# Kernel optimization log

Hardware: AMD Instinct MI355X
Metric: run time of the kernel (lower is better)

Reference implementation:

```python
import jax, jax.numpy as jnp
import numpy as np

B, L, D, H = 2, 2048, 1024, 16
DH = D // H  # 64

def setup_inputs() -> dict:
    key = jax.random.key(0)
    ks = jax.random.split(key, 5)
    s = 1.0 / np.sqrt(D)
    return {
        "x": jax.random.normal(ks[0], (B, L, D), jnp.float32),
        "Wk": jax.random.normal(ks[1], (D, D), jnp.float32) * s,
        "Wq": jax.random.normal(ks[2], (D, D), jnp.float32) * s,
        "Wv": jax.random.normal(ks[3], (D, D), jnp.float32) * s,
        "Wo": jax.random.normal(ks[4], (D, D), jnp.float32) * s,
    }

def reference(x, Wk, Wq, Wv, Wo):
    # Linear(D,D,bias=False): y = x @ W.T ; W stored [out,in] as in torch
    k = (x @ Wk.T).reshape(B, L, H, DH).transpose(0, 2, 1, 3)  # [B,H,L,dh]
    q = (x @ Wq.T).reshape(B, L, H, DH).transpose(0, 2, 1, 3)
    v = (x @ Wv.T).reshape(B, L, H, DH).transpose(0, 2, 1, 3)
    att = jnp.einsum("bhqd,bhkd->bhqk", q, k) / jnp.sqrt(jnp.float32(DH))
    causal = jnp.tril(jnp.ones((L, L), dtype=bool))
    att = jnp.where(causal, att, -jnp.inf)
    p = jax.nn.softmax(att, axis=-1)  # dropout omitted (eval mode)
    out = jnp.einsum("bhqk,bhkd->bhqd", p, v)  # [B,H,L,dh]
    out = out.transpose(0, 2, 1, 3).reshape(B, L, D)
    return out @ Wo.T
```

## Files before the change

kernel.cpp:

```cpp
#include <hip/hip_runtime.h>

typedef __bf16 bf16_t;
typedef __bf16 bf16x8 __attribute__((ext_vector_type(8)));
typedef __bf16 bf16x4 __attribute__((ext_vector_type(4)));
typedef float f32x4 __attribute__((ext_vector_type(4)));

#define MFMA_BF16(a, b, c) __builtin_amdgcn_mfma_f32_16x16x32_bf16((a), (b), (c), 0, 0, 0)

__device__ __forceinline__ void gload16(const bf16_t* g, bf16_t* l) {
  __builtin_amdgcn_global_load_lds(
      (__attribute__((address_space(1))) void*)(g),
      (__attribute__((address_space(3))) void*)(l), 16, 0, 0);
}

__global__ void cast_all(const float* __restrict__ x, const float* __restrict__ wk,
                         const float* __restrict__ wq, const float* __restrict__ wv,
                         const float* __restrict__ wo, bf16_t* __restrict__ xbf,
                         bf16_t* __restrict__ wbf) {
  const size_t NX = 4194304, NW = 1048576;
  size_t i = (size_t)blockIdx.x * blockDim.x + threadIdx.x;
  const size_t total4 = (NX + 4 * NW) / 4;
  const size_t stride = (size_t)gridDim.x * blockDim.x;
  for (; i < total4; i += stride) {
    size_t f = i * 4;
    const float* src;
    bf16_t* dst;
    if (f < NX) {
      src = x + f;
      dst = xbf + f;
    } else {
      size_t g = f - NX;
      size_t wsel = g >> 20;
      size_t off = g & (NW - 1);
      dst = wbf + g;
      src = (wsel == 0) ? wq + off : (wsel == 1) ? wk + off : (wsel == 2) ? wv + off : wo + off;
    }
    float4 v = *(const float4*)src;
    bf16x4 o;
    o[0] = (bf16_t)v.x; o[1] = (bf16_t)v.y; o[2] = (bf16_t)v.z; o[3] = (bf16_t)v.w;
    *(bf16x4*)dst = o;
  }
}

template <typename TOUT>
__global__ __launch_bounds__(256) void gemm_nt(const bf16_t* __restrict__ A,
                                               const bf16_t* __restrict__ W,
                                               TOUT* __restrict__ C, int K, int ldc,
                                               int blocksPerSect, bf16_t* __restrict__ vtb) {
  __shared__ bf16_t As[128 * 32];
  __shared__ bf16_t Bs[128 * 32];
  const int t = threadIdx.x;
  const int l = t & 63, w = t >> 6;
  const int wm = w >> 1, wn = w & 1;
  const int lr = l & 15, lg = l >> 4;
  const int bm = blockIdx.x;
  const int by = blockIdx.y;
  const int sect = by / blocksPerSect;
  const int bn = by - sect * blocksPerSect;
  const bf16_t* Wp = W + ((size_t)sect << 20);
  const int n0 = sect * 1024 + bn * 128;

  const bf16_t* ag = A + (size_t)(bm * 128 + (t >> 2)) * K + (t & 3) * 8;
  const bf16_t* bg = Wp + (size_t)(bn * 128 + (t >> 2)) * K + (t & 3) * 8;
  const size_t rs64 = (size_t)64 * K;

  f32x4 acc[4][4];
#pragma unroll
  for (int i = 0; i < 4; ++i)
#pragma unroll
    for (int j = 0; j < 4; ++j) acc[i][j] = (f32x4){0.f, 0.f, 0.f, 0.f};

  for (int k0 = 0; k0 < K; k0 += 32) {
    __syncthreads();
    gload16(ag, As + t * 8);
    gload16(ag + rs64, As + 2048 + t * 8);
    gload16(bg, Bs + t * 8);
    gload16(bg + rs64, Bs + 2048 + t * 8);
    ag += 32;
    bg += 32;
    __syncthreads();
    bf16x8 af[4], bfr[4];
#pragma unroll
    for (int mf = 0; mf < 4; ++mf)
      af[mf] = *(const bf16x8*)(As + (wm * 64 + mf * 16 + lr) * 32 + lg * 8);
#pragma unroll
    for (int nf = 0; nf < 4; ++nf)
      bfr[nf] = *(const bf16x8*)(Bs + (wn * 64 + nf * 16 + lr) * 32 + lg * 8);
#pragma unroll
    for (int mf = 0; mf < 4; ++mf)
#pragma unroll
      for (int nf = 0; nf < 4; ++nf)
        acc[mf][nf] = MFMA_BF16(af[mf], bfr[nf], acc[mf][nf]);
  }

  if (vtb != nullptr && sect == 2) {
#pragma unroll
    for (int mf = 0; mf < 4; ++mf)
#pragma unroll
      for (int nf = 0; nf < 4; ++nf) {
        int row0 = bm * 128 + wm * 64 + mf * 16 + lg * 4;
        int colg = bn * 128 + wn * 64 + nf * 16 + lr;
        int bb = row0 >> 11, ll = row0 & 2047;
        size_t vaddr = ((size_t)((bb * 16 + (colg >> 6)) * 64 + (colg & 63))) * 2048 + ll;
        bf16x4 pk;
#pragma unroll
        for (int j = 0; j < 4; ++j) pk[j] = (bf16_t)acc[mf][nf][j];
        *(bf16x4*)(vtb + vaddr) = pk;
      }
  } else {
#pragma unroll
    for (int mf = 0; mf < 4; ++mf)
#pragma unroll
      for (int nf = 0; nf < 4; ++nf)
#pragma unroll
        for (int j = 0; j < 4; ++j) {
          int row = bm * 128 + wm * 64 + mf * 16 + lg * 4 + j;
          int col = n0 + wn * 64 + nf * 16 + lr;
          C[(size_t)row * ldc + col] = (TOUT)acc[mf][nf][j];
        }
  }
}

__global__ __launch_bounds__(256) void attn_fwd(const bf16_t* __restrict__ qk,
                                                const bf16_t* __restrict__ vt,
                                                bf16_t* __restrict__ out) {
  __shared__ bf16_t Ks[64 * 64];
  __shared__ bf16_t Vts[64 * 64];
  __shared__ bf16_t Pt[4][16 * 72];
  const int t = threadIdx.x, l = t & 63, w = t >> 6;
  const int lr = l & 15, lg = l >> 4;
  const int bh = blockIdx.x;
  const int b = bh >> 4, h = bh & 15;
  const int qt = (int)(gridDim.y - 1) - (int)blockIdx.y;
  const int qrow = qt * 64 + w * 16 + lr;

  const bf16_t* Qg = qk + (size_t)(b * 2048 + qrow) * 2048 + h * 64 + lg * 8;
  bf16x8 qf0 = *(const bf16x8*)(Qg);
  bf16x8 qf1 = *(const bf16x8*)(Qg + 32);
#pragma unroll
  for (int j = 0; j < 8; ++j) {
    qf0[j] = (bf16_t)((float)qf0[j] * 0.125f);
    qf1[j] = (bf16_t)((float)qf1[j] * 0.125f);
  }

  f32x4 acc_o[4];
#pragma unroll
  for (int df = 0; df < 4; ++df) acc_o[df] = (f32x4){0.f, 0.f, 0.f, 0.f};
  float m_r = -1e30f, l_r = 0.f;
  bf16_t* Pw = &Pt[w][0];

  const int srow = t >> 3;
  const int sc8 = t & 7;

  for (int kt = 0; kt <= qt; ++kt) {
    __syncthreads();
#pragma unroll
    for (int r = 0; r < 2; ++r) {
      int row = r * 32 + srow;
      int cs = sc8 ^ (row & 7);
      gload16(qk + (size_t)(b * 2048 + kt * 64 + row) * 2048 + 1024 + h * 64 + cs * 8,
              Ks + (r * 256 + t) * 8);
      gload16(vt + ((size_t)(bh * 64 + row)) * 2048 + kt * 64 + cs * 8,
              Vts + (r * 256 + t) * 8);
    }
    __syncthreads();

    f32x4 sc[4];
#pragma unroll
    for (int nf = 0; nf < 4; ++nf) sc[nf] = (f32x4){0.f, 0.f, 0.f, 0.f};
#pragma unroll
    for (int nf = 0; nf < 4; ++nf) {
      int row = nf * 16 + lr;
      int r7 = row & 7;
      bf16x8 kf0 = *(const bf16x8*)(Ks + row * 64 + ((lg ^ r7) * 8));
      bf16x8 kf1 = *(const bf16x8*)(Ks + row * 64 + (((lg ^ 4) ^ r7) * 8));
      sc[nf] = MFMA_BF16(kf0, qf0, sc[nf]);
      sc[nf] = MFMA_BF16(kf1, qf1, sc[nf]);
    }
    float s[16];
#pragma unroll
    for (int nf = 0; nf < 4; ++nf)
#pragma unroll
      for (int j = 0; j < 4; ++j) s[nf * 4 + j] = sc[nf][j];
    if (kt == qt) {
      const int qloc = w * 16 + lr;
#pragma unroll
      for (int nf = 0; nf < 4; ++nf)
#pragma unroll
        for (int j = 0; j < 4; ++j)
          if (nf * 16 + lg * 4 + j > qloc) s[nf * 4 + j] = -1e30f;
    }

    float m16 = s[0];
#pragma unroll
    for (int i = 1; i < 16; ++i) m16 = fmaxf(m16, s[i]);
    float rm = fmaxf(m16, __shfl_xor(m16, 16));
    rm = fmaxf(rm, __shfl_xor(rm, 32));
    float mnew = fmaxf(m_r, rm);
    float sf = __expf(m_r - mnew);
    m_r = mnew;
    float p[16], ps = 0.f;
#pragma unroll
    for (int i = 0; i < 16; ++i) {
      p[i] = __expf(s[i] - mnew);
      ps += p[i];
    }
    ps += __shfl_xor(ps, 16);
    ps += __shfl_xor(ps, 32);
    l_r = l_r * sf + ps;
#pragma unroll
    for (int df = 0; df < 4; ++df)
#pragma unroll
      for (int j = 0; j < 4; ++j) acc_o[df][j] *= sf;

#pragma unroll
    for (int nf = 0; nf < 4; ++nf) {
      bf16x4 pk;
#pragma unroll
      for (int j = 0; j < 4; ++j) pk[j] = (bf16_t)p[nf * 4 + j];
      *(bf16x4*)(Pw + lr * 72 + nf * 16 + lg * 4) = pk;
    }

    bf16x8 pb0 = *(const bf16x8*)(Pw + lr * 72 + lg * 8);
    bf16x8 pb1 = *(const bf16x8*)(Pw + lr * 72 + 32 + lg * 8);
#pragma unroll
    for (int df = 0; df < 4; ++df) {
      int arow = df * 16 + lr;
      int r7 = arow & 7;
      bf16x8 vf0 = *(const bf16x8*)(Vts + arow * 64 + ((lg ^ r7) * 8));
      bf16x8 vf1 = *(const bf16x8*)(Vts + arow * 64 + (((lg ^ 4) ^ r7) * 8));
      acc_o[df] = MFMA_BF16(vf0, pb0, acc_o[df]);
      acc_o[df] = MFMA_BF16(vf1, pb1, acc_o[df]);
    }
  }

  float inv = 1.f / l_r;
#pragma unroll
  for (int df = 0; df < 4; ++df) {
    bf16x4 o;
#pragma unroll
    for (int j = 0; j < 4; ++j) o[j] = (bf16_t)(acc_o[df][j] * inv);
    *(bf16x4*)(out + (size_t)(b * 2048 + qrow) * 1024 + h * 64 + df * 16 + lg * 4) = o;
  }
}

extern "C" void kernel_launch(void* const* d_in, const int* in_sizes, int n_in,
                              void* d_out, int out_size, void* d_ws, size_t ws_size,
                              hipStream_t stream) {
  const float* x = (const float*)d_in[0];
  const float* wk = (const float*)d_in[1];
  const float* wq = (const float*)d_in[2];
  const float* wv = (const float*)d_in[3];
  const float* wo = (const float*)d_in[4];

  bf16_t* xbf = (bf16_t*)d_ws;
  bf16_t* wbf = xbf + 4194304;
  bf16_t* qkbf = wbf + 4194304;
  bf16_t* vtbuf = qkbf + 8388608;
  bf16_t* attnbf = xbf;
  float* out = (float*)d_out;

  cast_all<<<dim3(2048), dim3(256), 0, stream>>>(x, wk, wq, wv, wo, xbf, wbf);
  gemm_nt<bf16_t><<<dim3(32, 24), dim3(256), 0, stream>>>(xbf, wbf, qkbf, 1024, 2048, 8, vtbuf);
  attn_fwd<<<dim3(32, 32), dim3(256), 0, stream>>>(qkbf, vtbuf, attnbf);
  gemm_nt<float><<<dim3(32, 8), dim3(256), 0, stream>>>(attnbf, wbf + 3 * 1048576, out, 1024,
                                                        1024, 8, (bf16_t*)nullptr);
}
```

Measured before the change: 120.1 us.

## Pair causal query tiles per block, double-buffer K/V, and lazily rescale softmax

Each attention block now handles two query tiles (qt and 31-qt), so every block does the same amount of causal work and K/V tiles loaded into LDS serve both query tiles while they overlap. K/V loads are double-buffered so the next tile's global-to-LDS copy runs during the current tile's compute, with one barrier per iteration instead of two. The online softmax skips rescaling the accumulators unless the row max grows by more than a threshold. The trade-off is half as many blocks, with more registers and LDS per block.

```diff
diff --git a/kernel.cpp b/kernel.cpp
--- a/kernel.cpp
+++ b/kernel.cpp
@@ -121,126 +121,174 @@
   }
 }
 
+template <int NP>
+__device__ __forceinline__ void attn_tile(const bf16_t* Kb, const bf16_t* Vb, bf16_t* Pw,
+                                          const bf16x8 (&qf)[2][2], f32x4 (&acc)[2][4],
+                                          float (&m_r)[2], float (&l_r)[2], int qloc,
+                                          const int (&diag)[2], int lr, int lg) {
+  f32x4 sc[2][4];
+#pragma unroll
+  for (int pp = 0; pp < NP; ++pp)
+#pragma unroll
+    for (int nf = 0; nf < 4; ++nf) sc[pp][nf] = (f32x4){0.f, 0.f, 0.f, 0.f};
+#pragma unroll
+  for (int nf = 0; nf < 4; ++nf) {
+    int row = nf * 16 + lr, r7 = row & 7;
+    bf16x8 kf0 = *(const bf16x8*)(Kb + row * 64 + (lg ^ r7) * 8);
+    bf16x8 kf1 = *(const bf16x8*)(Kb + row * 64 + ((lg ^ 4) ^ r7) * 8);
+#pragma unroll
+    for (int pp = 0; pp < NP; ++pp) {
+      sc[pp][nf] = MFMA_BF16(kf0, qf[pp][0], sc[pp][nf]);
+      sc[pp][nf] = MFMA_BF16(kf1, qf[pp][1], sc[pp][nf]);
+    }
+  }
+#pragma unroll
+  for (int pp = 0; pp < NP; ++pp) {
+    float s[16];
+#pragma unroll
+    for (int nf = 0; nf < 4; ++nf)
+#pragma unroll
+      for (int j = 0; j < 4; ++j) s[nf * 4 + j] = sc[pp][nf][j];
+    if (diag[pp]) {
+#pragma unroll
+      for (int nf = 0; nf < 4; ++nf)
+#pragma unroll
+        for (int j = 0; j < 4; ++j)
+          if (nf * 16 + lg * 4 + j > qloc) s[nf * 4 + j] = -1e30f;
+    }
+    float t0 = fmaxf(fmaxf(s[0], s[1]), fmaxf(s[2], s[3]));
+    float t1 = fmaxf(fmaxf(s[4], s[5]), fmaxf(s[6], s[7]));
+    float t2 = fmaxf(fmaxf(s[8], s[9]), fmaxf(s[10], s[11]));
+    float t3 = fmaxf(fmaxf(s[12], s[13]), fmaxf(s[14], s[15]));
+    float m16 = fmaxf(fmaxf(t0, t1), fmaxf(t2, t3));
+    float rm = fmaxf(m16, __shfl_xor(m16, 16));
+    rm = fmaxf(rm, __shfl_xor(rm, 32));
+    if (!__all(rm - m_r[pp] <= 8.f)) {
+      float mnew = fmaxf(m_r[pp], rm);
+      float sf = __expf(m_r[pp] - mnew);
+      m_r[pp] = mnew;
+      l_r[pp] *= sf;
+#pragma unroll
+      for (int df = 0; df < 4; ++df)
+#pragma unroll
+        for (int j = 0; j < 4; ++j) acc[pp][df][j] *= sf;
+    }
+    float p[16], ps = 0.f;
+#pragma unroll
+    for (int i = 0; i < 16; ++i) {
+      p[i] = __expf(s[i] - m_r[pp]);
+      ps += p[i];
+    }
+    ps += __shfl_xor(ps, 16);
+    ps += __shfl_xor(ps, 32);
+    l_r[pp] += ps;
+#pragma unroll
+    for (int nf = 0; nf < 4; ++nf) {
+      bf16x4 pk;
+#pragma unroll
+      for (int j = 0; j < 4; ++j) pk[j] = (bf16_t)p[nf * 4 + j];
+      *(bf16x4*)(Pw + pp * 1152 + lr * 72 + nf * 16 + lg * 4) = pk;
+    }
+  }
+  bf16x8 pb[2][2];
+#pragma unroll
+  for (int pp = 0; pp < NP; ++pp) {
+    pb[pp][0] = *(const bf16x8*)(Pw + pp * 1152 + lr * 72 + lg * 8);
+    pb[pp][1] = *(const bf16x8*)(Pw + pp * 1152 + lr * 72 + 32 + lg * 8);
+  }
+#pragma unroll
+  for (int df = 0; df < 4; ++df) {
+    int arow = df * 16 + lr, r7 = arow & 7;
+    bf16x8 vf0 = *(const bf16x8*)(Vb + arow * 64 + (lg ^ r7) * 8);
+    bf16x8 vf1 = *(const bf16x8*)(Vb + arow * 64 + ((lg ^ 4) ^ r7) * 8);
+#pragma unroll
+    for (int pp = 0; pp < NP; ++pp) {
+      acc[pp][df] = MFMA_BF16(vf0, pb[pp][0], acc[pp][df]);
+      acc[pp][df] = MFMA_BF16(vf1, pb[pp][1], acc[pp][df]);
+    }
+  }
+}
+
 __global__ __launch_bounds__(256) void attn_fwd(const bf16_t* __restrict__ qk,
                                                 const bf16_t* __restrict__ vt,
                                                 bf16_t* __restrict__ out) {
-  __shared__ bf16_t Ks[64 * 64];
-  __shared__ bf16_t Vts[64 * 64];
-  __shared__ bf16_t Pt[4][16 * 72];
+  __shared__ bf16_t Ks[2][4096];
+  __shared__ bf16_t Vts[2][4096];
+  __shared__ bf16_t Pt[4][2304];
   const int t = threadIdx.x, l = t & 63, w = t >> 6;
   const int lr = l & 15, lg = l >> 4;
   const int bh = blockIdx.x;
   const int b = bh >> 4, h = bh & 15;
-  const int qt = (int)(gridDim.y - 1) - (int)blockIdx.y;
-  const int qrow = qt * 64 + w * 16 + lr;
-
-  const bf16_t* Qg = qk + (size_t)(b * 2048 + qrow) * 2048 + h * 64 + lg * 8;
-  bf16x8 qf0 = *(const bf16x8*)(Qg);
-  bf16x8 qf1 = *(const bf16x8*)(Qg + 32);
-#pragma unroll
-  for (int j = 0; j < 8; ++j) {
-    qf0[j] = (bf16_t)((float)qf0[j] * 0.125f);
-    qf1[j] = (bf16_t)((float)qf1[j] * 0.125f);
-  }
-
-  f32x4 acc_o[4];
-#pragma unroll
-  for (int df = 0; df < 4; ++df) acc_o[df] = (f32x4){0.f, 0.f, 0.f, 0.f};
-  float m_r = -1e30f, l_r = 0.f;
+  const int pr = blockIdx.y;
+  const int qlo = pr, qhi = 31 - pr;
+  const int qtile[2] = {qhi, qlo};
+  const int qloc = w * 16 + lr;
+
+  const int srow = t >> 3, sc8 = t & 7;
+  const int cs = sc8 ^ (srow & 7);
+  const bf16_t* kbase = qk + ((size_t)(b * 2048 + srow)) * 2048 + 1024 + h * 64 + cs * 8;
+  const bf16_t* vbase = vt + ((size_t)(bh * 64 + srow)) * 2048 + cs * 8;
   bf16_t* Pw = &Pt[w][0];
 
-  const int srow = t >> 3;
-  const int sc8 = t & 7;
-
-  for (int kt = 0; kt <= qt; ++kt) {
+#define STAGE(ktile, buf)                                              \
+  do {                                                                 \
+    const bf16_t* ks_ = kbase + (size_t)(ktile) * (64 * 2048);         \
+    const bf16_t* vs_ = vbase + (size_t)(ktile) * 64;                  \
+    gload16(ks_, &Ks[buf][t * 8]);                                     \
+    gload16(ks_ + (size_t)32 * 2048, &Ks[buf][2048 + t * 8]);          \
+    gload16(vs_, &Vts[buf][t * 8]);                                    \
+    gload16(vs_ + (size_t)32 * 2048, &Vts[buf][2048 + t * 8]);         \
+  } while (0)
+
+  bf16x8 qf[2][2];
+#pragma unroll
+  for (int pp = 0; pp < 2; ++pp) {
+    const bf16_t* Qg =
+        qk + (size_t)(b * 2048 + qtile[pp] * 64 + w * 16 + lr) * 2048 + h * 64 + lg * 8;
+    qf[pp][0] = *(const bf16x8*)(Qg);
+    qf[pp][1] = *(const bf16x8*)(Qg + 32);
+#pragma unroll
+    for (int j = 0; j < 8; ++j) {
+      qf[pp][0][j] = (bf16_t)((float)qf[pp][0][j] * 0.125f);
+      qf[pp][1][j] = (bf16_t)((float)qf[pp][1][j] * 0.125f);
+    }
+  }
+
+  f32x4 acc[2][4];
+#pragma unroll
+  for (int pp = 0; pp < 2; ++pp)
+#pragma unroll
+    for (int df = 0; df < 4; ++df) acc[pp][df] = (f32x4){0.f, 0.f, 0.f, 0.f};
+  float m_r[2] = {-1e30f, -1e30f};
+  float l_r[2] = {0.f, 0.f};
+
+  STAGE(0, 0);
+  __syncthreads();
+
+  int cur = 0;
+  for (int kt = 0; kt <= qhi; ++kt) {
+    if (kt < qhi) STAGE(kt + 1, cur ^ 1);
+    const int diag[2] = {kt == qhi, kt == qlo};
+    if (kt <= qlo)
+      attn_tile<2>(&Ks[cur][0], &Vts[cur][0], Pw, qf, acc, m_r, l_r, qloc, diag, lr, lg);
+    else
+      attn_tile<1>(&Ks[cur][0], &Vts[cur][0], Pw, qf, acc, m_r, l_r, qloc, diag, lr, lg);
     __syncthreads();
-#pragma unroll
-    for (int r = 0; r < 2; ++r) {
-      int row = r * 32 + srow;
-      int cs = sc8 ^ (row & 7);
-      gload16(qk + (size_t)(b * 2048 + kt * 64 + row) * 2048 + 1024 + h * 64 + cs * 8,
-              Ks + (r * 256 + t) * 8);
-      gload16(vt + ((size_t)(bh * 64 + row)) * 2048 + kt * 64 + cs * 8,
-              Vts + (r * 256 + t) * 8);
-    }
-    __syncthreads();
-
-    f32x4 sc[4];
-#pragma unroll
-    for (int nf = 0; nf < 4; ++nf) sc[nf] = (f32x4){0.f, 0.f, 0.f, 0.f};
-#pragma unroll
-    for (int nf = 0; nf < 4; ++nf) {
-      int row = nf * 16 + lr;
-      int r7 = row & 7;
-      bf16x8 kf0 = *(const bf16x8*)(Ks + row * 64 + ((lg ^ r7) * 8));
-      bf16x8 kf1 = *(const bf16x8*)(Ks + row * 64 + (((lg ^ 4) ^ r7) * 8));
-      sc[nf] = MFMA_BF16(kf0, qf0, sc[nf]);
-      sc[nf] = MFMA_BF16(kf1, qf1, sc[nf]);
-    }
-    float s[16];
-#pragma unroll
-    for (int nf = 0; nf < 4; ++nf)
-#pragma unroll
-      for (int j = 0; j < 4; ++j) s[nf * 4 + j] = sc[nf][j];
-    if (kt == qt) {
-      const int qloc = w * 16 + lr;
-#pragma unroll
-      for (int nf = 0; nf < 4; ++nf)
-#pragma unroll
-        for (int j = 0; j < 4; ++j)
-          if (nf * 16 + lg * 4 + j > qloc) s[nf * 4 + j] = -1e30f;
-    }
-
-    float m16 = s[0];
-#pragma unroll
-    for (int i = 1; i < 16; ++i) m16 = fmaxf(m16, s[i]);
-    float rm = fmaxf(m16, __shfl_xor(m16, 16));
-    rm = fmaxf(rm, __shfl_xor(rm, 32));
-    float mnew = fmaxf(m_r, rm);
-    float sf = __expf(m_r - mnew);
-    m_r = mnew;
-    float p[16], ps = 0.f;
-#pragma unroll
-    for (int i = 0; i < 16; ++i) {
-      p[i] = __expf(s[i] - mnew);
-      ps += p[i];
-    }
-    ps += __shfl_xor(ps, 16);
-    ps += __shfl_xor(ps, 32);
-    l_r = l_r * sf + ps;
-#pragma unroll
-    for (int df = 0; df < 4; ++df)
-#pragma unroll
-      for (int j = 0; j < 4; ++j) acc_o[df][j] *= sf;
-
-#pragma unroll
-    for (int nf = 0; nf < 4; ++nf) {
-      bf16x4 pk;
-#pragma unroll
-      for (int j = 0; j < 4; ++j) pk[j] = (bf16_t)p[nf * 4 + j];
-      *(bf16x4*)(Pw + lr * 72 + nf * 16 + lg * 4) = pk;
-    }
-
-    bf16x8 pb0 = *(const bf16x8*)(Pw + lr * 72 + lg * 8);
-    bf16x8 pb1 = *(const bf16x8*)(Pw + lr * 72 + 32 + lg * 8);
+    cur ^= 1;
+  }
+#undef STAGE
+
+#pragma unroll
+  for (int pp = 0; pp < 2; ++pp) {
+    float inv = 1.f / l_r[pp];
+    int qrow = qtile[pp] * 64 + w * 16 + lr;
 #pragma unroll
     for (int df = 0; df < 4; ++df) {
-      int arow = df * 16 + lr;
-      int r7 = arow & 7;
-      bf16x8 vf0 = *(const bf16x8*)(Vts + arow * 64 + ((lg ^ r7) * 8));
-      bf16x8 vf1 = *(const bf16x8*)(Vts + arow * 64 + (((lg ^ 4) ^ r7) * 8));
-      acc_o[df] = MFMA_BF16(vf0, pb0, acc_o[df]);
-      acc_o[df] = MFMA_BF16(vf1, pb1, acc_o[df]);
-    }
-  }
-
-  float inv = 1.f / l_r;
-#pragma unroll
-  for (int df = 0; df < 4; ++df) {
-    bf16x4 o;
-#pragma unroll
-    for (int j = 0; j < 4; ++j) o[j] = (bf16_t)(acc_o[df][j] * inv);
-    *(bf16x4*)(out + (size_t)(b * 2048 + qrow) * 1024 + h * 64 + df * 16 + lg * 4) = o;
+      bf16x4 o;
+#pragma unroll
+      for (int j = 0; j < 4; ++j) o[j] = (bf16_t)(acc[pp][df][j] * inv);
+      *(bf16x4*)(out + (size_t)(b * 2048 + qrow) * 1024 + h * 64 + df * 16 + lg * 4) = o;
+    }
   }
 }
 
@@ -262,7 +310,7 @@
 
   cast_all<<<dim3(2048), dim3(256), 0, stream>>>(x, wk, wq, wv, wo, xbf, wbf);
   gemm_nt<bf16_t><<<dim3(32, 24), dim3(256), 0, stream>>>(xbf, wbf, qkbf, 1024, 2048, 8, vtbuf);
-  attn_fwd<<<dim3(32, 32), dim3(256), 0, stream>>>(qkbf, vtbuf, attnbf);
+  attn_fwd<<<dim3(32, 16), dim3(256), 0, stream>>>(qkbf, vtbuf, attnbf);
   gemm_nt<float><<<dim3(32, 8), dim3(256), 0, stream>>>(attnbf, wbf + 3 * 1048576, out, 1024,
                                                         1024, 8, (bf16_t*)nullptr);
 }
```

Measured after the change: 124.1 us. +3.4%, slower.

## Double-buffer K/V tiles in attention and add lazy softmax rescaling

Applied to the files above, without the earlier changes.

The attention kernel now prefetches the next K/V tile into a second LDS buffer while computing on the current one, using one barrier per iteration instead of two. It also switches exp to exp2 with folded log2e, skips rescaling of the accumulator unless the running max grows by more than a threshold, swizzles the P scratch buffer to avoid bank conflicts, and raises wave priority around the MFMA sections. LDS use doubles for K/V, and the lazy-rescale threshold lets exponent values exceed 1 temporarily, which relies on fp32 headroom.

```diff
diff --git a/kernel.cpp b/kernel.cpp
--- a/kernel.cpp
+++ b/kernel.cpp
@@ -6,6 +6,7 @@
 typedef float f32x4 __attribute__((ext_vector_type(4)));
 
 #define MFMA_BF16(a, b, c) __builtin_amdgcn_mfma_f32_16x16x32_bf16((a), (b), (c), 0, 0, 0)
+#define LOG2E 1.44269504088896f
 
 __device__ __forceinline__ void gload16(const bf16_t* g, bf16_t* l) {
   __builtin_amdgcn_global_load_lds(
@@ -124,15 +125,31 @@
 __global__ __launch_bounds__(256) void attn_fwd(const bf16_t* __restrict__ qk,
                                                 const bf16_t* __restrict__ vt,
                                                 bf16_t* __restrict__ out) {
-  __shared__ bf16_t Ks[64 * 64];
-  __shared__ bf16_t Vts[64 * 64];
-  __shared__ bf16_t Pt[4][16 * 72];
+  __shared__ bf16_t Ks[2][4096];
+  __shared__ bf16_t Vts[2][4096];
+  __shared__ bf16_t Pt[4][1024];
   const int t = threadIdx.x, l = t & 63, w = t >> 6;
   const int lr = l & 15, lg = l >> 4;
   const int bh = blockIdx.x;
   const int b = bh >> 4, h = bh & 15;
-  const int qt = (int)(gridDim.y - 1) - (int)blockIdx.y;
-  const int qrow = qt * 64 + w * 16 + lr;
+  const int qt = 31 - (int)blockIdx.y;
+  const int qloc = w * 16 + lr;
+  const int qrow = qt * 64 + qloc;
+
+  const int srow = t >> 3, sc8 = t & 7;
+  const int cs = sc8 ^ (srow & 7);
+  const bf16_t* kbase = qk + ((size_t)(b * 2048 + srow)) * 2048 + 1024 + h * 64 + cs * 8;
+  const bf16_t* vbase = vt + ((size_t)(bh * 64 + srow)) * 2048 + cs * 8;
+
+#define STAGE(ktile, buf)                                              \
+  do {                                                                 \
+    const bf16_t* ks_ = kbase + (size_t)(ktile) * (64 * 2048);         \
+    const bf16_t* vs_ = vbase + (size_t)(ktile) * 64;                  \
+    gload16(ks_, &Ks[buf][t * 8]);                                     \
+    gload16(ks_ + (size_t)32 * 2048, &Ks[buf][2048 + t * 8]);          \
+    gload16(vs_, &Vts[buf][t * 8]);                                    \
+    gload16(vs_ + (size_t)32 * 2048, &Vts[buf][2048 + t * 8]);         \
+  } while (0)
 
   const bf16_t* Qg = qk + (size_t)(b * 2048 + qrow) * 2048 + h * 64 + lg * 8;
   bf16x8 qf0 = *(const bf16x8*)(Qg);
@@ -143,47 +160,41 @@
     qf1[j] = (bf16_t)((float)qf1[j] * 0.125f);
   }
 
-  f32x4 acc_o[4];
-#pragma unroll
-  for (int df = 0; df < 4; ++df) acc_o[df] = (f32x4){0.f, 0.f, 0.f, 0.f};
+  f32x4 acc[4];
+#pragma unroll
+  for (int df = 0; df < 4; ++df) acc[df] = (f32x4){0.f, 0.f, 0.f, 0.f};
   float m_r = -1e30f, l_r = 0.f;
-  bf16_t* Pw = &Pt[w][0];
-
-  const int srow = t >> 3;
-  const int sc8 = t & 7;
-
+
+  char* PwB = (char*)&Pt[w][0];
+  const int psw = (lr & 7) << 4;
+
+  STAGE(0, 0);
+  __syncthreads();
+
+  int cur = 0;
   for (int kt = 0; kt <= qt; ++kt) {
-    __syncthreads();
-#pragma unroll
-    for (int r = 0; r < 2; ++r) {
-      int row = r * 32 + srow;
-      int cs = sc8 ^ (row & 7);
-      gload16(qk + (size_t)(b * 2048 + kt * 64 + row) * 2048 + 1024 + h * 64 + cs * 8,
-              Ks + (r * 256 + t) * 8);
-      gload16(vt + ((size_t)(bh * 64 + row)) * 2048 + kt * 64 + cs * 8,
-              Vts + (r * 256 + t) * 8);
-    }
-    __syncthreads();
+    if (kt < qt) STAGE(kt + 1, cur ^ 1);
 
     f32x4 sc[4];
 #pragma unroll
     for (int nf = 0; nf < 4; ++nf) sc[nf] = (f32x4){0.f, 0.f, 0.f, 0.f};
+    __builtin_amdgcn_s_setprio(1);
 #pragma unroll
     for (int nf = 0; nf < 4; ++nf) {
-      int row = nf * 16 + lr;
-      int r7 = row & 7;
-      bf16x8 kf0 = *(const bf16x8*)(Ks + row * 64 + ((lg ^ r7) * 8));
-      bf16x8 kf1 = *(const bf16x8*)(Ks + row * 64 + (((lg ^ 4) ^ r7) * 8));
+      int row = nf * 16 + lr, r7 = row & 7;
+      bf16x8 kf0 = *(const bf16x8*)(&Ks[cur][row * 64 + (lg ^ r7) * 8]);
+      bf16x8 kf1 = *(const bf16x8*)(&Ks[cur][row * 64 + ((lg ^ 4) ^ r7) * 8]);
       sc[nf] = MFMA_BF16(kf0, qf0, sc[nf]);
       sc[nf] = MFMA_BF16(kf1, qf1, sc[nf]);
     }
+    __builtin_amdgcn_s_setprio(0);
+
     float s[16];
 #pragma unroll
     for (int nf = 0; nf < 4; ++nf)
 #pragma unroll
       for (int j = 0; j < 4; ++j) s[nf * 4 + j] = sc[nf][j];
     if (kt == qt) {
-      const int qloc = w * 16 + lr;
 #pragma unroll
       for (int nf = 0; nf < 4; ++nf)
 #pragma unroll
@@ -191,55 +202,65 @@
           if (nf * 16 + lg * 4 + j > qloc) s[nf * 4 + j] = -1e30f;
     }
 
-    float m16 = s[0];
-#pragma unroll
-    for (int i = 1; i < 16; ++i) m16 = fmaxf(m16, s[i]);
+    float t0 = fmaxf(fmaxf(s[0], s[1]), fmaxf(s[2], s[3]));
+    float t1 = fmaxf(fmaxf(s[4], s[5]), fmaxf(s[6], s[7]));
+    float t2 = fmaxf(fmaxf(s[8], s[9]), fmaxf(s[10], s[11]));
+    float t3 = fmaxf(fmaxf(s[12], s[13]), fmaxf(s[14], s[15]));
+    float m16 = fmaxf(fmaxf(t0, t1), fmaxf(t2, t3));
     float rm = fmaxf(m16, __shfl_xor(m16, 16));
     rm = fmaxf(rm, __shfl_xor(rm, 32));
-    float mnew = fmaxf(m_r, rm);
-    float sf = __expf(m_r - mnew);
-    m_r = mnew;
+    if (!__all(rm - m_r <= 8.f)) {
+      float mnew = fmaxf(m_r, rm);
+      float sf = __builtin_amdgcn_exp2f((m_r - mnew) * LOG2E);
+      m_r = mnew;
+      l_r *= sf;
+#pragma unroll
+      for (int df = 0; df < 4; ++df)
+#pragma unroll
+        for (int j = 0; j < 4; ++j) acc[df][j] *= sf;
+    }
+    const float m2 = m_r * LOG2E;
     float p[16], ps = 0.f;
 #pragma unroll
     for (int i = 0; i < 16; ++i) {
-      p[i] = __expf(s[i] - mnew);
+      p[i] = __builtin_amdgcn_exp2f(fmaf(s[i], LOG2E, -m2));
       ps += p[i];
     }
     ps += __shfl_xor(ps, 16);
     ps += __shfl_xor(ps, 32);
-    l_r = l_r * sf + ps;
-#pragma unroll
-    for (int df = 0; df < 4; ++df)
-#pragma unroll
-      for (int j = 0; j < 4; ++j) acc_o[df][j] *= sf;
+    l_r += ps;
 
 #pragma unroll
     for (int nf = 0; nf < 4; ++nf) {
       bf16x4 pk;
 #pragma unroll
       for (int j = 0; j < 4; ++j) pk[j] = (bf16_t)p[nf * 4 + j];
-      *(bf16x4*)(Pw + lr * 72 + nf * 16 + lg * 4) = pk;
-    }
-
-    bf16x8 pb0 = *(const bf16x8*)(Pw + lr * 72 + lg * 8);
-    bf16x8 pb1 = *(const bf16x8*)(Pw + lr * 72 + 32 + lg * 8);
+      *(bf16x4*)(PwB + lr * 128 + ((nf * 32 + lg * 8) ^ psw)) = pk;
+    }
+
+    bf16x8 pb0 = *(const bf16x8*)(PwB + lr * 128 + ((lg * 16) ^ psw));
+    bf16x8 pb1 = *(const bf16x8*)(PwB + lr * 128 + ((64 + lg * 16) ^ psw));
+    __builtin_amdgcn_s_setprio(1);
 #pragma unroll
     for (int df = 0; df < 4; ++df) {
-      int arow = df * 16 + lr;
-      int r7 = arow & 7;
-      bf16x8 vf0 = *(const bf16x8*)(Vts + arow * 64 + ((lg ^ r7) * 8));
-      bf16x8 vf1 = *(const bf16x8*)(Vts + arow * 64 + (((lg ^ 4) ^ r7) * 8));
-      acc_o[df] = MFMA_BF16(vf0, pb0, acc_o[df]);
-      acc_o[df] = MFMA_BF16(vf1, pb1, acc_o[df]);
-    }
-  }
+      int arow = df * 16 + lr, r7 = arow & 7;
+      bf16x8 vf0 = *(const bf16x8*)(&Vts[cur][arow * 64 + (lg ^ r7) * 8]);
+      bf16x8 vf1 = *(const bf16x8*)(&Vts[cur][arow * 64 + ((lg ^ 4) ^ r7) * 8]);
+      acc[df] = MFMA_BF16(vf0, pb0, acc[df]);
+      acc[df] = MFMA_BF16(vf1, pb1, acc[df]);
+    }
+    __builtin_amdgcn_s_setprio(0);
+    __syncthreads();
+    cur ^= 1;
+  }
+#undef STAGE
 
   float inv = 1.f / l_r;
 #pragma unroll
   for (int df = 0; df < 4; ++df) {
     bf16x4 o;
 #pragma unroll
-    for (int j = 0; j < 4; ++j) o[j] = (bf16_t)(acc_o[df][j] * inv);
+    for (int j = 0; j < 4; ++j) o[j] = (bf16_t)(acc[df][j] * inv);
     *(bf16x4*)(out + (size_t)(b * 2048 + qrow) * 1024 + h * 64 + df * 16 + lg * 4) = o;
   }
 }
```

Measured after the change: 120.7 us. No clear change (+0.5%).
